# Kernel tuning notes

Hardware: AMD Instinct MI355X
Metric: run time of the kernel (lower is better)

## Reference

```python
import jax, jax.numpy as jnp
import numpy as np

ITERS = 3

def squash(s, axis):
    # v = (|s|^2 / (1 + |s|^2)) * s / |s|
    sn = jnp.sum(s * s, axis=axis, keepdims=True)
    return sn / (1.0 + sn) * s / jnp.sqrt(sn)

def setup_inputs() -> dict:
    key = jax.random.key(0)
    k1, k2 = jax.random.split(key)
    b, B, C, P2, f = 8, 144, 16, 16, 12
    u = jax.random.normal(k1, (b, B, C, P2, f, f), dtype=jnp.float32)
    a = jax.random.uniform(k2, (b, B, f, f), dtype=jnp.float32)
    return {"u": u, "a": a}

def reference(u, a):
    # u: (b, B, C, P2, f, f); a: (b, B, f, f)
    b, B, C, P2, f, _ = u.shape
    # r: (b, B, C, 1, f, f), initialized uniform over C scaled by activation
    r = jnp.broadcast_to(a[:, :, None, None, :, :] * (1.0 / C), (b, B, C, 1, f, f))
    v = None
    for i in range(ITERS):
        c = jax.nn.softmax(r, axis=2)                       # over C
        v = squash(jnp.sum(c * u, axis=1, keepdims=True), axis=3)  # (b,1,C,P2,f,f)
        if i != ITERS - 1:
            r = r + jnp.sum(u * v, axis=3, keepdims=True)   # agreement over psize
    a_out = jnp.sqrt(jnp.sum(v * v, axis=3, keepdims=True))  # (b,1,C,1,f,f)
    return (jnp.squeeze(v, axis=1), jnp.squeeze(a_out, axis=(1, 3)))
```

## Files before the change

### kernel.cpp

```cpp
#include <hip/hip_runtime.h>
#include <math.h>


#define NB 8
#define BDIM 144
#define CDIM 16
#define PDIM 16
#define SDIM 144
#define NF4 (SDIM / 4)
#define BC 8
#define WJ (BC / 4)
#define NPT 9
#define NBC (BDIM / BC)
#define UF4STRIDE ((size_t)CDIM * PDIM * NF4)
#define VELEMS (NB * CDIM * PDIM * SDIM)
#define VF4 (VELEMS / 4)

static __device__ __forceinline__ float4 f4zero() {
  return make_float4(0.f, 0.f, 0.f, 0.f);
}
static __device__ __forceinline__ float4 f4add(float4 a, float4 b) {
  return make_float4(a.x + b.x, a.y + b.y, a.z + b.z, a.w + b.w);
}
static __device__ __forceinline__ float4 f4fma(float4 a, float4 b, float4 c) {
  return make_float4(fmaf(a.x, b.x, c.x), fmaf(a.y, b.y, c.y),
                     fmaf(a.z, b.z, c.z), fmaf(a.w, b.w, c.w));
}
static __device__ __forceinline__ float4 f4scale(float4 a, float s) {
  return make_float4(a.x * s, a.y * s, a.z * s, a.w * s);
}

__global__ __launch_bounds__(256, 2) void route_f4(
    const float* __restrict__ u, const float* __restrict__ a,
    const float* __restrict__ V, float* __restrict__ part, int iter) {
  __shared__ float4 comb[2][64][PDIM + 1];

  const int tid = threadIdx.x;
  const int w = tid >> 6;
  const int lane = tid & 63;
  const int c = lane >> 2;
  const int posq = lane & 3;
  const int chunk = blockIdx.x;
  const int y = blockIdx.y;
  const int b = blockIdx.z;
  const int f4 = y * 4 + posq;
  const int B0 = chunk * BC + w * WJ;

  const float4* ub =
      (const float4*)u + ((size_t)((b * BDIM + B0) * CDIM + c) * PDIM) * NF4 + f4;

  float4 sacc[PDIM];
#pragma unroll
  for (int p = 0; p < PDIM; ++p) sacc[p] = f4zero();

  if (iter == 0) {
#pragma unroll
    for (int jj = 0; jj < WJ; ++jj) {
      const float4* up = ub + (size_t)jj * UF4STRIDE;
#pragma unroll
      for (int p = 0; p < PDIM; ++p) sacc[p] = f4add(sacc[p], up[p * NF4]);
    }
  } else {
    float4 Vr[PDIM];
    {
      const float4* vb =
          (const float4*)V + ((size_t)(b * CDIM + c) * PDIM) * NF4 + f4;
#pragma unroll
      for (int p = 0; p < PDIM; ++p) Vr[p] = vb[p * NF4];
    }
#pragma unroll
    for (int jj = 0; jj < WJ; ++jj) {
      const float4* up = ub + (size_t)jj * UF4STRIDE;
      float4 uu[PDIM];
#pragma unroll
      for (int p = 0; p < PDIM; ++p) uu[p] = up[p * NF4];
      const float4 av =
          ((const float4*)(a + (size_t)(b * BDIM + B0 + jj) * SDIM))[f4];
      float4 dot = f4scale(av, 1.0f / CDIM);
#pragma unroll
      for (int p = 0; p < PDIM; ++p) dot = f4fma(uu[p], Vr[p], dot);
      float4 e;
      e.x = __expf(dot.x); e.y = __expf(dot.y);
      e.z = __expf(dot.z); e.w = __expf(dot.w);
      float4 se = e;
#pragma unroll
      for (int m = 4; m <= 32; m <<= 1) {
        se.x += __shfl_xor(se.x, m);
        se.y += __shfl_xor(se.y, m);
        se.z += __shfl_xor(se.z, m);
        se.w += __shfl_xor(se.w, m);
      }
      float4 wg;
      wg.x = e.x * __builtin_amdgcn_rcpf(se.x);
      wg.y = e.y * __builtin_amdgcn_rcpf(se.y);
      wg.z = e.z * __builtin_amdgcn_rcpf(se.z);
      wg.w = e.w * __builtin_amdgcn_rcpf(se.w);
#pragma unroll
      for (int p = 0; p < PDIM; ++p) sacc[p] = f4fma(wg, uu[p], sacc[p]);
    }
  }

  if (w >= 2) {
#pragma unroll
    for (int p = 0; p < PDIM; ++p) comb[w - 2][lane][p] = sacc[p];
  }
  __syncthreads();
  if (w < 2) {
#pragma unroll
    for (int p = 0; p < PDIM; ++p) sacc[p] = f4add(sacc[p], comb[w][lane][p]);
  }
  __syncthreads();
  if (w == 1) {
#pragma unroll
    for (int p = 0; p < PDIM; ++p) comb[0][lane][p] = sacc[p];
  }
  __syncthreads();
  if (w == 0) {
#pragma unroll
    for (int p = 0; p < PDIM; ++p) sacc[p] = f4add(sacc[p], comb[0][lane][p]);
    const float sc = (iter == 0) ? (1.0f / CDIM) : 1.0f;
    float4* sp = (float4*)part + (size_t)chunk * VF4 +
                 ((size_t)(b * CDIM + c) * PDIM) * NF4 + f4;
#pragma unroll
    for (int p = 0; p < PDIM; ++p) sp[p * NF4] = f4scale(sacc[p], sc);
  }
}

__global__ __launch_bounds__(256) void reduce_f4(
    const float* __restrict__ part, float* __restrict__ V,
    float* __restrict__ out_v, float* __restrict__ out_a, int iter) {
  const int tid = threadIdx.x;
  const int w = tid >> 6;
  const int lane = tid & 63;
  const int p = lane >> 2;
  const int posq = lane & 3;
  const int quad = blockIdx.x;
  const int c = blockIdx.y * 4 + w;
  const int b = blockIdx.z;
  const int f4 = quad * 4 + posq;
  const size_t idx = ((size_t)((b * CDIM + c) * PDIM) + p) * NF4 + f4;

  float4 sv = f4zero();
#pragma unroll
  for (int k = 0; k < NBC; ++k)
    sv = f4add(sv, ((const float4*)part)[(size_t)k * VF4 + idx]);

  float4 sn = make_float4(sv.x * sv.x, sv.y * sv.y, sv.z * sv.z, sv.w * sv.w);
#pragma unroll
  for (int m = 4; m <= 32; m <<= 1) {
    sn.x += __shfl_xor(sn.x, m);
    sn.y += __shfl_xor(sn.y, m);
    sn.z += __shfl_xor(sn.z, m);
    sn.w += __shfl_xor(sn.w, m);
  }
  float4 sc;
  sc.x = sn.x / (1.0f + sn.x) * rsqrtf(sn.x);
  sc.y = sn.y / (1.0f + sn.y) * rsqrtf(sn.y);
  sc.z = sn.z / (1.0f + sn.z) * rsqrtf(sn.z);
  sc.w = sn.w / (1.0f + sn.w) * rsqrtf(sn.w);

  float4* Vb = (float4*)V + idx;
  if (iter == 0) {
    *Vb = make_float4(sv.x * sc.x, sv.y * sc.y, sv.z * sc.z, sv.w * sc.w);
  } else if (iter == 1) {
    float4 o = *Vb;
    *Vb = make_float4(fmaf(sv.x, sc.x, o.x), fmaf(sv.y, sc.y, o.y),
                      fmaf(sv.z, sc.z, o.z), fmaf(sv.w, sc.w, o.w));
  } else {
    ((float4*)out_v)[idx] =
        make_float4(sv.x * sc.x, sv.y * sc.y, sv.z * sc.z, sv.w * sc.w);
    if (p == 0) {
      ((float4*)out_a)[(size_t)(b * CDIM + c) * NF4 + f4] =
          make_float4(sn.x / (1.0f + sn.x), sn.y / (1.0f + sn.y),
                      sn.z / (1.0f + sn.z), sn.w / (1.0f + sn.w));
    }
  }
}


extern "C" void kernel_launch(void* const* d_in, const int* in_sizes, int n_in,
                              void* d_out, int out_size, void* d_ws, size_t ws_size,
                              hipStream_t stream) {
  const float* u = (const float*)d_in[0];
  const float* a = (const float*)d_in[1];
  float* out_v = (float*)d_out;
  float* out_a = out_v + VELEMS;

  float* V = (float*)d_ws;
  float* part = V + VELEMS;

  const dim3 gR(NBC, NPT, NB);
  const dim3 gQ(NPT, 4, NB);
  for (int it = 0; it < 3; ++it) {
    route_f4<<<gR, 256, 0, stream>>>(u, a, V, part, it);
    reduce_f4<<<gQ, 256, 0, stream>>>(part, V, out_v, out_a, it);
  }
}
```

Measured before the change: 374.6 us.

## Cache fp16-packed copy of u in first pass and read it in later iterations

```diff
diff --git a/kernel.cpp b/kernel.cpp
--- a/kernel.cpp
+++ b/kernel.cpp
@@ -1,4 +1,5 @@
 #include <hip/hip_runtime.h>
+#include <hip/hip_fp16.h>
 #include <math.h>
 
 
@@ -9,12 +10,13 @@
 #define SDIM 144
 #define NF4 (SDIM / 4)
 #define BC 8
-#define WJ (BC / 4)
+#define WJ 2
+#define NBC (BDIM / BC)
 #define NPT 9
-#define NBC (BDIM / BC)
 #define UF4STRIDE ((size_t)CDIM * PDIM * NF4)
 #define VELEMS (NB * CDIM * PDIM * SDIM)
 #define VF4 (VELEMS / 4)
+#define U16Q_PER_B ((size_t)NF4 * 8 * CDIM)
 
 static __device__ __forceinline__ float4 f4zero() {
   return make_float4(0.f, 0.f, 0.f, 0.f);
@@ -22,17 +24,20 @@
 static __device__ __forceinline__ float4 f4add(float4 a, float4 b) {
   return make_float4(a.x + b.x, a.y + b.y, a.z + b.z, a.w + b.w);
 }
-static __device__ __forceinline__ float4 f4fma(float4 a, float4 b, float4 c) {
-  return make_float4(fmaf(a.x, b.x, c.x), fmaf(a.y, b.y, c.y),
-                     fmaf(a.z, b.z, c.z), fmaf(a.w, b.w, c.w));
-}
-static __device__ __forceinline__ float4 f4scale(float4 a, float s) {
-  return make_float4(a.x * s, a.y * s, a.z * s, a.w * s);
-}
-
-__global__ __launch_bounds__(256, 2) void route_f4(
-    const float* __restrict__ u, const float* __restrict__ a,
-    const float* __restrict__ V, float* __restrict__ part, int iter) {
+static __device__ __forceinline__ unsigned pk16(float lo, float hi) {
+  union { __half2 h; unsigned u; } v;
+  v.h = __floats2half2_rn(lo, hi);
+  return v.u;
+}
+static __device__ __forceinline__ float2 upk16(unsigned x) {
+  union { __half2 h; unsigned u; } v;
+  v.u = x;
+  return __half22float2(v.h);
+}
+
+__global__ __launch_bounds__(256) void capsA(
+    const float* __restrict__ u, uint4* __restrict__ u16q,
+    float* __restrict__ part) {
   __shared__ float4 comb[2][64][PDIM + 1];
 
   const int tid = threadIdx.x;
@@ -43,60 +48,143 @@
   const int chunk = blockIdx.x;
   const int y = blockIdx.y;
   const int b = blockIdx.z;
-  const int f4 = y * 4 + posq;
+  const int f4i = y * 4 + posq;
   const int B0 = chunk * BC + w * WJ;
 
   const float4* ub =
-      (const float4*)u + ((size_t)((b * BDIM + B0) * CDIM + c) * PDIM) * NF4 + f4;
+      (const float4*)u + ((size_t)((b * BDIM + B0) * CDIM + c) * PDIM) * NF4 + f4i;
 
   float4 sacc[PDIM];
 #pragma unroll
   for (int p = 0; p < PDIM; ++p) sacc[p] = f4zero();
 
-  if (iter == 0) {
-#pragma unroll
-    for (int jj = 0; jj < WJ; ++jj) {
-      const float4* up = ub + (size_t)jj * UF4STRIDE;
-#pragma unroll
-      for (int p = 0; p < PDIM; ++p) sacc[p] = f4add(sacc[p], up[p * NF4]);
-    }
-  } else {
-    float4 Vr[PDIM];
+#pragma unroll
+  for (int jj = 0; jj < WJ; ++jj) {
+    const float4* ubj = ub + (size_t)jj * UF4STRIDE;
+    uint4* uq = u16q + ((size_t)(b * BDIM + B0 + jj) * NF4 + f4i) * (8 * CDIM) + c;
+#pragma unroll
+    for (int p2 = 0; p2 < 8; ++p2) {
+      const float4 lo = ubj[(2 * p2) * NF4];
+      const float4 hi = ubj[(2 * p2 + 1) * NF4];
+      sacc[2 * p2] = f4add(sacc[2 * p2], lo);
+      sacc[2 * p2 + 1] = f4add(sacc[2 * p2 + 1], hi);
+      uq[p2 * CDIM] =
+          make_uint4(pk16(lo.x, hi.x), pk16(lo.y, hi.y),
+                     pk16(lo.z, hi.z), pk16(lo.w, hi.w));
+    }
+  }
+
+  if (w >= 2) {
+#pragma unroll
+    for (int p = 0; p < PDIM; ++p) comb[w - 2][lane][p] = sacc[p];
+  }
+  __syncthreads();
+  if (w < 2) {
+#pragma unroll
+    for (int p = 0; p < PDIM; ++p) sacc[p] = f4add(sacc[p], comb[w][lane][p]);
+  }
+  __syncthreads();
+  if (w == 1) {
+#pragma unroll
+    for (int p = 0; p < PDIM; ++p) comb[0][lane][p] = sacc[p];
+  }
+  __syncthreads();
+  if (w == 0) {
+    float4* sp = (float4*)part + (size_t)chunk * VF4 +
+                 ((size_t)(b * CDIM + c) * PDIM) * NF4 + f4i;
+#pragma unroll
+    for (int p = 0; p < PDIM; ++p) {
+      const float4 v = f4add(sacc[p], comb[0][lane][p]);
+      sp[p * NF4] = make_float4(v.x * (1.0f / CDIM), v.y * (1.0f / CDIM),
+                                v.z * (1.0f / CDIM), v.w * (1.0f / CDIM));
+    }
+  }
+}
+
+__global__ __launch_bounds__(256) void capsB(
+    const uint4* __restrict__ u16q, const float* __restrict__ a,
+    const float* __restrict__ V, float* __restrict__ part) {
+  __shared__ float4 comb[2][64][PDIM + 1];
+
+  const int tid = threadIdx.x;
+  const int w = tid >> 6;
+  const int lane = tid & 63;
+  const int c = lane >> 2;
+  const int posq = lane & 3;
+  const int chunk = blockIdx.x;
+  const int y = blockIdx.y;
+  const int b = blockIdx.z;
+  const int f4i = y * 4 + posq;
+  const int B0 = chunk * BC + w * WJ;
+
+  float4 Vr[PDIM];
+  {
+    const float4* vb =
+        (const float4*)V + ((size_t)(b * CDIM + c) * PDIM) * NF4 + f4i;
+#pragma unroll
+    for (int p = 0; p < PDIM; ++p) Vr[p] = vb[p * NF4];
+  }
+
+  float4 sacc[PDIM];
+#pragma unroll
+  for (int p = 0; p < PDIM; ++p) sacc[p] = f4zero();
+
+#pragma unroll
+  for (int jj = 0; jj < WJ; ++jj) {
+    const uint4* uq =
+        u16q + ((size_t)(b * BDIM + B0 + jj) * NF4 + f4i) * (8 * CDIM) + c;
+    uint4 U[8];
+#pragma unroll
+    for (int p2 = 0; p2 < 8; ++p2) U[p2] = uq[p2 * CDIM];
+
+    float4 dot;
     {
-      const float4* vb =
-          (const float4*)V + ((size_t)(b * CDIM + c) * PDIM) * NF4 + f4;
-#pragma unroll
-      for (int p = 0; p < PDIM; ++p) Vr[p] = vb[p * NF4];
-    }
-#pragma unroll
-    for (int jj = 0; jj < WJ; ++jj) {
-      const float4* up = ub + (size_t)jj * UF4STRIDE;
-      float4 uu[PDIM];
-#pragma unroll
-      for (int p = 0; p < PDIM; ++p) uu[p] = up[p * NF4];
       const float4 av =
-          ((const float4*)(a + (size_t)(b * BDIM + B0 + jj) * SDIM))[f4];
-      float4 dot = f4scale(av, 1.0f / CDIM);
-#pragma unroll
-      for (int p = 0; p < PDIM; ++p) dot = f4fma(uu[p], Vr[p], dot);
-      float4 e;
-      e.x = __expf(dot.x); e.y = __expf(dot.y);
-      e.z = __expf(dot.z); e.w = __expf(dot.w);
-      float4 se = e;
-#pragma unroll
-      for (int m = 4; m <= 32; m <<= 1) {
-        se.x += __shfl_xor(se.x, m);
-        se.y += __shfl_xor(se.y, m);
-        se.z += __shfl_xor(se.z, m);
-        se.w += __shfl_xor(se.w, m);
-      }
-      float4 wg;
-      wg.x = e.x * __builtin_amdgcn_rcpf(se.x);
-      wg.y = e.y * __builtin_amdgcn_rcpf(se.y);
-      wg.z = e.z * __builtin_amdgcn_rcpf(se.z);
-      wg.w = e.w * __builtin_amdgcn_rcpf(se.w);
-#pragma unroll
-      for (int p = 0; p < PDIM; ++p) sacc[p] = f4fma(wg, uu[p], sacc[p]);
+          ((const float4*)(a + (size_t)(b * BDIM + B0 + jj) * SDIM))[f4i];
+      dot = make_float4(av.x * (1.0f / CDIM), av.y * (1.0f / CDIM),
+                        av.z * (1.0f / CDIM), av.w * (1.0f / CDIM));
+    }
+#pragma unroll
+    for (int p2 = 0; p2 < 8; ++p2) {
+      const float4 va = Vr[2 * p2];
+      const float4 vb2 = Vr[2 * p2 + 1];
+      const float2 t0 = upk16(U[p2].x);
+      const float2 t1 = upk16(U[p2].y);
+      const float2 t2 = upk16(U[p2].z);
+      const float2 t3 = upk16(U[p2].w);
+      dot.x = fmaf(t0.x, va.x, fmaf(t0.y, vb2.x, dot.x));
+      dot.y = fmaf(t1.x, va.y, fmaf(t1.y, vb2.y, dot.y));
+      dot.z = fmaf(t2.x, va.z, fmaf(t2.y, vb2.z, dot.z));
+      dot.w = fmaf(t3.x, va.w, fmaf(t3.y, vb2.w, dot.w));
+    }
+    float4 e;
+    e.x = __expf(dot.x); e.y = __expf(dot.y);
+    e.z = __expf(dot.z); e.w = __expf(dot.w);
+    float4 se = e;
+#pragma unroll
+    for (int m = 4; m <= 32; m <<= 1) {
+      se.x += __shfl_xor(se.x, m);
+      se.y += __shfl_xor(se.y, m);
+      se.z += __shfl_xor(se.z, m);
+      se.w += __shfl_xor(se.w, m);
+    }
+    float4 w4;
+    w4.x = e.x * __builtin_amdgcn_rcpf(se.x);
+    w4.y = e.y * __builtin_amdgcn_rcpf(se.y);
+    w4.z = e.z * __builtin_amdgcn_rcpf(se.z);
+    w4.w = e.w * __builtin_amdgcn_rcpf(se.w);
+#pragma unroll
+    for (int p2 = 0; p2 < 8; ++p2) {
+      float4& sa = sacc[2 * p2];
+      float4& sb = sacc[2 * p2 + 1];
+      const float2 t0 = upk16(U[p2].x);
+      const float2 t1 = upk16(U[p2].y);
+      const float2 t2 = upk16(U[p2].z);
+      const float2 t3 = upk16(U[p2].w);
+      sa.x = fmaf(w4.x, t0.x, sa.x); sb.x = fmaf(w4.x, t0.y, sb.x);
+      sa.y = fmaf(w4.y, t1.x, sa.y); sb.y = fmaf(w4.y, t1.y, sb.y);
+      sa.z = fmaf(w4.z, t2.x, sa.z); sb.z = fmaf(w4.z, t2.y, sb.z);
+      sa.w = fmaf(w4.w, t3.x, sa.w); sb.w = fmaf(w4.w, t3.y, sb.w);
     }
   }
 
@@ -116,13 +204,11 @@
   }
   __syncthreads();
   if (w == 0) {
-#pragma unroll
-    for (int p = 0; p < PDIM; ++p) sacc[p] = f4add(sacc[p], comb[0][lane][p]);
-    const float sc = (iter == 0) ? (1.0f / CDIM) : 1.0f;
     float4* sp = (float4*)part + (size_t)chunk * VF4 +
-                 ((size_t)(b * CDIM + c) * PDIM) * NF4 + f4;
-#pragma unroll
-    for (int p = 0; p < PDIM; ++p) sp[p * NF4] = f4scale(sacc[p], sc);
+                 ((size_t)(b * CDIM + c) * PDIM) * NF4 + f4i;
+#pragma unroll
+    for (int p = 0; p < PDIM; ++p)
+      sp[p * NF4] = f4add(sacc[p], comb[0][lane][p]);
   }
 }
 
@@ -188,11 +274,15 @@
 
   float* V = (float*)d_ws;
   float* part = V + VELEMS;
+  uint4* u16q = (uint4*)(part + (size_t)NBC * VELEMS);
 
   const dim3 gR(NBC, NPT, NB);
   const dim3 gQ(NPT, 4, NB);
-  for (int it = 0; it < 3; ++it) {
-    route_f4<<<gR, 256, 0, stream>>>(u, a, V, part, it);
-    reduce_f4<<<gQ, 256, 0, stream>>>(part, V, out_v, out_a, it);
-  }
-}
+
+  capsA<<<gR, 256, 0, stream>>>(u, u16q, part);
+  reduce_f4<<<gQ, 256, 0, stream>>>(part, V, out_v, out_a, 0);
+  capsB<<<gR, 256, 0, stream>>>(u16q, a, V, part);
+  reduce_f4<<<gQ, 256, 0, stream>>>(part, V, out_v, out_a, 1);
+  capsB<<<gR, 256, 0, stream>>>(u16q, a, V, part);
+  reduce_f4<<<gQ, 256, 0, stream>>>(part, V, out_v, out_a, 2);
+}
```

Measured after the change: 332.9 us. 11.1% less time.

## Cache u as fp16 during first pass and read it in later routing passes

Applied to the files above, without the earlier changes.

```diff
diff --git a/kernel.cpp b/kernel.cpp
--- a/kernel.cpp
+++ b/kernel.cpp
@@ -1,4 +1,5 @@
 #include <hip/hip_runtime.h>
+#include <hip/hip_fp16.h>
 #include <math.h>
 
 
@@ -9,12 +10,12 @@
 #define SDIM 144
 #define NF4 (SDIM / 4)
 #define BC 8
-#define WJ (BC / 4)
+#define WJ 2
+#define NBC (BDIM / BC)
 #define NPT 9
-#define NBC (BDIM / BC)
-#define UF4STRIDE ((size_t)CDIM * PDIM * NF4)
 #define VELEMS (NB * CDIM * PDIM * SDIM)
 #define VF4 (VELEMS / 4)
+#define A1THREADS (NBC * NB * CDIM * PDIM * NF4)
 
 static __device__ __forceinline__ float4 f4zero() {
   return make_float4(0.f, 0.f, 0.f, 0.f);
@@ -22,17 +23,52 @@
 static __device__ __forceinline__ float4 f4add(float4 a, float4 b) {
   return make_float4(a.x + b.x, a.y + b.y, a.z + b.z, a.w + b.w);
 }
-static __device__ __forceinline__ float4 f4fma(float4 a, float4 b, float4 c) {
-  return make_float4(fmaf(a.x, b.x, c.x), fmaf(a.y, b.y, c.y),
-                     fmaf(a.z, b.z, c.z), fmaf(a.w, b.w, c.w));
-}
-static __device__ __forceinline__ float4 f4scale(float4 a, float s) {
-  return make_float4(a.x * s, a.y * s, a.z * s, a.w * s);
-}
-
-__global__ __launch_bounds__(256, 2) void route_f4(
-    const float* __restrict__ u, const float* __restrict__ a,
-    const float* __restrict__ V, float* __restrict__ part, int iter) {
+static __device__ __forceinline__ unsigned pk16(float lo, float hi) {
+  union { __half2 h; unsigned u; } v;
+  v.h = __floats2half2_rn(lo, hi);
+  return v.u;
+}
+static __device__ __forceinline__ float2 upk16(unsigned x) {
+  union { __half2 h; unsigned u; } v;
+  v.u = x;
+  return __half22float2(v.h);
+}
+
+__global__ __launch_bounds__(256) void capsA1(
+    const float* __restrict__ u, uint2* __restrict__ u16,
+    float* __restrict__ part) {
+  const int o = blockIdx.x * 256 + threadIdx.x;
+  const int f4 = o % NF4;
+  const int r1 = o / NF4;
+  const int cp = r1 & 255;
+  const int r2 = r1 >> 8;
+  const int b = r2 & 7;
+  const int chunk = r2 >> 3;
+
+  const float4* ub = (const float4*)u +
+                     ((size_t)(b * BDIM + chunk * BC) * 256 + cp) * NF4 + f4;
+  uint2* uq = u16 + ((size_t)(b * BDIM + chunk * BC) * 256 + cp) * NF4 + f4;
+
+  float4 v[BC];
+#pragma unroll
+  for (int j = 0; j < BC; ++j)
+    v[j] = ub[(size_t)j * (256 * NF4)];
+
+  float4 s = f4zero();
+#pragma unroll
+  for (int j = 0; j < BC; ++j) {
+    s = f4add(s, v[j]);
+    uq[(size_t)j * (256 * NF4)] =
+        make_uint2(pk16(v[j].x, v[j].y), pk16(v[j].z, v[j].w));
+  }
+  ((float4*)part)[(size_t)chunk * VF4 + (size_t)(b * 256 + cp) * NF4 + f4] =
+      make_float4(s.x * (1.0f / CDIM), s.y * (1.0f / CDIM),
+                  s.z * (1.0f / CDIM), s.w * (1.0f / CDIM));
+}
+
+__global__ __launch_bounds__(256) void capsB(
+    const uint2* __restrict__ u16, const float* __restrict__ a,
+    const float* __restrict__ V, float* __restrict__ part) {
   __shared__ float4 comb[2][64][PDIM + 1];
 
   const int tid = threadIdx.x;
@@ -43,60 +79,69 @@
   const int chunk = blockIdx.x;
   const int y = blockIdx.y;
   const int b = blockIdx.z;
-  const int f4 = y * 4 + posq;
+  const int f4i = y * 4 + posq;
   const int B0 = chunk * BC + w * WJ;
 
-  const float4* ub =
-      (const float4*)u + ((size_t)((b * BDIM + B0) * CDIM + c) * PDIM) * NF4 + f4;
+  float4 Vr[PDIM];
+  {
+    const float4* vb =
+        (const float4*)V + ((size_t)(b * CDIM + c) * PDIM) * NF4 + f4i;
+#pragma unroll
+    for (int p = 0; p < PDIM; ++p) Vr[p] = vb[p * NF4];
+  }
 
   float4 sacc[PDIM];
 #pragma unroll
   for (int p = 0; p < PDIM; ++p) sacc[p] = f4zero();
 
-  if (iter == 0) {
-#pragma unroll
-    for (int jj = 0; jj < WJ; ++jj) {
-      const float4* up = ub + (size_t)jj * UF4STRIDE;
-#pragma unroll
-      for (int p = 0; p < PDIM; ++p) sacc[p] = f4add(sacc[p], up[p * NF4]);
-    }
-  } else {
-    float4 Vr[PDIM];
+#pragma unroll
+  for (int jj = 0; jj < WJ; ++jj) {
+    const uint2* uq =
+        u16 + ((size_t)(b * BDIM + B0 + jj) * 256 + c * PDIM) * NF4 + f4i;
+    uint2 U[PDIM];
+#pragma unroll
+    for (int p = 0; p < PDIM; ++p) U[p] = uq[p * NF4];
+
+    float4 dot;
     {
-      const float4* vb =
-          (const float4*)V + ((size_t)(b * CDIM + c) * PDIM) * NF4 + f4;
-#pragma unroll
-      for (int p = 0; p < PDIM; ++p) Vr[p] = vb[p * NF4];
-    }
-#pragma unroll
-    for (int jj = 0; jj < WJ; ++jj) {
-      const float4* up = ub + (size_t)jj * UF4STRIDE;
-      float4 uu[PDIM];
-#pragma unroll
-      for (int p = 0; p < PDIM; ++p) uu[p] = up[p * NF4];
       const float4 av =
-          ((const float4*)(a + (size_t)(b * BDIM + B0 + jj) * SDIM))[f4];
-      float4 dot = f4scale(av, 1.0f / CDIM);
-#pragma unroll
-      for (int p = 0; p < PDIM; ++p) dot = f4fma(uu[p], Vr[p], dot);
-      float4 e;
-      e.x = __expf(dot.x); e.y = __expf(dot.y);
-      e.z = __expf(dot.z); e.w = __expf(dot.w);
-      float4 se = e;
-#pragma unroll
-      for (int m = 4; m <= 32; m <<= 1) {
-        se.x += __shfl_xor(se.x, m);
-        se.y += __shfl_xor(se.y, m);
-        se.z += __shfl_xor(se.z, m);
-        se.w += __shfl_xor(se.w, m);
-      }
-      float4 wg;
-      wg.x = e.x * __builtin_amdgcn_rcpf(se.x);
-      wg.y = e.y * __builtin_amdgcn_rcpf(se.y);
-      wg.z = e.z * __builtin_amdgcn_rcpf(se.z);
-      wg.w = e.w * __builtin_amdgcn_rcpf(se.w);
-#pragma unroll
-      for (int p = 0; p < PDIM; ++p) sacc[p] = f4fma(wg, uu[p], sacc[p]);
+          ((const float4*)(a + (size_t)(b * BDIM + B0 + jj) * SDIM))[f4i];
+      dot = make_float4(av.x * (1.0f / CDIM), av.y * (1.0f / CDIM),
+                        av.z * (1.0f / CDIM), av.w * (1.0f / CDIM));
+    }
+#pragma unroll
+    for (int p = 0; p < PDIM; ++p) {
+      const float2 t01 = upk16(U[p].x);
+      const float2 t23 = upk16(U[p].y);
+      dot.x = fmaf(t01.x, Vr[p].x, dot.x);
+      dot.y = fmaf(t01.y, Vr[p].y, dot.y);
+      dot.z = fmaf(t23.x, Vr[p].z, dot.z);
+      dot.w = fmaf(t23.y, Vr[p].w, dot.w);
+    }
+    float4 e;
+    e.x = __expf(dot.x); e.y = __expf(dot.y);
+    e.z = __expf(dot.z); e.w = __expf(dot.w);
+    float4 se = e;
+#pragma unroll
+    for (int m = 4; m <= 32; m <<= 1) {
+      se.x += __shfl_xor(se.x, m);
+      se.y += __shfl_xor(se.y, m);
+      se.z += __shfl_xor(se.z, m);
+      se.w += __shfl_xor(se.w, m);
+    }
+    float4 w4;
+    w4.x = e.x * __builtin_amdgcn_rcpf(se.x);
+    w4.y = e.y * __builtin_amdgcn_rcpf(se.y);
+    w4.z = e.z * __builtin_amdgcn_rcpf(se.z);
+    w4.w = e.w * __builtin_amdgcn_rcpf(se.w);
+#pragma unroll
+    for (int p = 0; p < PDIM; ++p) {
+      const float2 t01 = upk16(U[p].x);
+      const float2 t23 = upk16(U[p].y);
+      sacc[p].x = fmaf(w4.x, t01.x, sacc[p].x);
+      sacc[p].y = fmaf(w4.y, t01.y, sacc[p].y);
+      sacc[p].z = fmaf(w4.z, t23.x, sacc[p].z);
+      sacc[p].w = fmaf(w4.w, t23.y, sacc[p].w);
     }
   }
 
@@ -116,13 +161,11 @@
   }
   __syncthreads();
   if (w == 0) {
-#pragma unroll
-    for (int p = 0; p < PDIM; ++p) sacc[p] = f4add(sacc[p], comb[0][lane][p]);
-    const float sc = (iter == 0) ? (1.0f / CDIM) : 1.0f;
     float4* sp = (float4*)part + (size_t)chunk * VF4 +
-                 ((size_t)(b * CDIM + c) * PDIM) * NF4 + f4;
-#pragma unroll
-    for (int p = 0; p < PDIM; ++p) sp[p * NF4] = f4scale(sacc[p], sc);
+                 ((size_t)(b * CDIM + c) * PDIM) * NF4 + f4i;
+#pragma unroll
+    for (int p = 0; p < PDIM; ++p)
+      sp[p * NF4] = f4add(sacc[p], comb[0][lane][p]);
   }
 }
 
@@ -188,11 +231,15 @@
 
   float* V = (float*)d_ws;
   float* part = V + VELEMS;
+  uint2* u16 = (uint2*)(part + (size_t)NBC * VELEMS);
 
   const dim3 gR(NBC, NPT, NB);
   const dim3 gQ(NPT, 4, NB);
-  for (int it = 0; it < 3; ++it) {
-    route_f4<<<gR, 256, 0, stream>>>(u, a, V, part, it);
-    reduce_f4<<<gQ, 256, 0, stream>>>(part, V, out_v, out_a, it);
-  }
-}
+
+  capsA1<<<A1THREADS / 256, 256, 0, stream>>>(u, u16, part);
+  reduce_f4<<<gQ, 256, 0, stream>>>(part, V, out_v, out_a, 0);
+  capsB<<<gR, 256, 0, stream>>>(u16, a, V, part);
+  reduce_f4<<<gQ, 256, 0, stream>>>(part, V, out_v, out_a, 1);
+  capsB<<<gR, 256, 0, stream>>>(u16, a, V, part);
+  reduce_f4<<<gQ, 256, 0, stream>>>(part, V, out_v, out_a, 2);
+}
```

Measured after the change: 376.3 us. Within noise of the previous version (+0.4%).
